# Kernel optimization log

Measured on AMD Instinct MI355X. Metric: run time of the kernel, lower is better.

## Reference

```python
import jax, jax.numpy as jnp
import numpy as np

N_NODES = 50000
SEQ_LEN = 32
N_TOKENS = 100000
EMB_DIM = 128          # in_feats / 2
IN_FEATS = 256
N_HIDDEN = 256
N_CLASSES = 40
N_EDGES = 800000
PAD_IX = 0


def setup_inputs() -> dict:
    key = jax.random.key(0)
    k1, k2, k3, k4, k5, k6 = jax.random.split(key, 6)
    features = jax.random.randint(k1, (N_NODES, SEQ_LEN), 0, N_TOKENS, dtype=jnp.int32)
    src = jax.random.randint(k2, (N_EDGES,), 0, N_NODES, dtype=jnp.int32)
    dst = jax.random.randint(k3, (N_EDGES,), 0, N_NODES, dtype=jnp.int32)
    emb_table = jax.random.normal(k4, (N_TOKENS, EMB_DIM), dtype=jnp.float32) * 0.02
    W1 = jax.random.normal(k5, (IN_FEATS, N_HIDDEN), dtype=jnp.float32) * 0.02
    b1 = jnp.zeros((N_HIDDEN,), dtype=jnp.float32)
    W2 = jax.random.normal(k6, (N_HIDDEN, N_CLASSES), dtype=jnp.float32) * 0.02
    b2 = jnp.zeros((N_CLASSES,), dtype=jnp.float32)
    return {"features": features, "src": src, "dst": dst,
            "emb_table": emb_table, "W1": W1, "b1": b1, "W2": W2, "b2": b2}


def _apply_embs(features, emb_table):
    # padding_idx row contributes zeros (nn.Embedding padding_idx semantics)
    emb = emb_table.at[PAD_IX].set(0.0)
    h = emb[features]                                    # [N, L, D]
    seq_len = jnp.sum(features != PAD_IX, axis=1)        # [N]
    seq_len = jnp.maximum(seq_len, 1)[:, None].astype(h.dtype)
    h1 = h.sum(axis=1) / seq_len                         # masked mean
    h2 = h.max(axis=1)                                   # max pool (pads are 0)
    return jnp.concatenate((h1, h2), axis=1)             # [N, 2D]


def _graph_conv(h, src, dst, norm_s, norm_d, W, b):
    # DGL GraphConv, norm='both': out = D_in^{-1/2} A D_out^{-1/2} h W + b
    hw = h @ W                                           # transform first (smaller msgs)
    m = (hw * norm_s[:, None])[src]                      # gather messages [E, F]
    agg = jax.ops.segment_sum(m, dst, num_segments=N_NODES)
    return agg * norm_d[:, None] + b


def reference(features, src, dst, emb_table, W1, b1, W2, b2):
    ones_e = jnp.ones((src.shape[0],), dtype=jnp.float32)
    deg_out = jnp.maximum(jax.ops.segment_sum(ones_e, src, num_segments=N_NODES), 1.0)
    deg_in = jnp.maximum(jax.ops.segment_sum(ones_e, dst, num_segments=N_NODES), 1.0)
    norm_s = deg_out ** -0.5
    norm_d = deg_in ** -0.5

    h = _apply_embs(features, emb_table)                 # [N, in_feats]
    h = jax.nn.relu(_graph_conv(h, src, dst, norm_s, norm_d, W1, b1))
    # dropout is identity in eval mode
    h = _graph_conv(h, src, dst, norm_s, norm_d, W2, b2)
    return h                                             # [N, n_classes]
```

## Files before the change

kernel.cpp:

```cpp
#include <hip/hip_runtime.h>
#include <math.h>

#define N_NODES 50000
#define SEQ_LEN 32
#define EMB_DIM 128
#define IN_FEATS 256
#define N_HIDDEN 256
#define N_CLASSES 40
#define N_EDGES 800000
#define N_TOKENS 100000

#define SLOT 64
#define NBIN 196
#define BINCAP 4608
#define EPB 4000

typedef short short8 __attribute__((ext_vector_type(8)));
typedef float f32x4 __attribute__((ext_vector_type(4)));
typedef float f32x8 __attribute__((ext_vector_type(8)));

__device__ __forceinline__ unsigned short f2bf(float x) {
  unsigned int u = __float_as_uint(x);
  unsigned int r = (u + 0x7FFFu + ((u >> 16) & 1u)) >> 16;
  return (unsigned short)r;
}
__device__ __forceinline__ float bf2f(unsigned short s) {
  return __uint_as_float((unsigned int)s << 16);
}
__device__ __forceinline__ unsigned int pack2bf(float a, float b) {
  return (unsigned int)f2bf(a) | ((unsigned int)f2bf(b) << 16);
}
__device__ __forceinline__ f32x8 up8(uint4 v) {
  f32x8 f;
  f[0] = __uint_as_float(v.x << 16);
  f[1] = __uint_as_float(v.x & 0xFFFF0000u);
  f[2] = __uint_as_float(v.y << 16);
  f[3] = __uint_as_float(v.y & 0xFFFF0000u);
  f[4] = __uint_as_float(v.z << 16);
  f[5] = __uint_as_float(v.z & 0xFFFF0000u);
  f[6] = __uint_as_float(v.w << 16);
  f[7] = __uint_as_float(v.w & 0xFFFF0000u);
  return f;
}

__global__ __launch_bounds__(256) void k_pre(const int* __restrict__ src,
                                             const int* __restrict__ dst,
                                             int* __restrict__ gcntD,
                                             int* __restrict__ gcntS,
                                             unsigned int* __restrict__ dbin,
                                             unsigned char* __restrict__ sbin,
                                             const float* __restrict__ emb,
                                             unsigned short* __restrict__ emb_b,
                                             const float* __restrict__ W1,
                                             unsigned short* __restrict__ Wp1,
                                             const float* __restrict__ W2,
                                             unsigned short* __restrict__ Wp2) {
  __shared__ int cntD[NBIN], cntS[NBIN], baseD[NBIN], baseS[NBIN];
  int b = blockIdx.x, tid = threadIdx.x;
  if (b < 200) {
    if (tid < NBIN) { cntD[tid] = 0; cntS[tid] = 0; }
    __syncthreads();
    int e0 = b * EPB;
    for (int j = tid; j < EPB; j += 256) {
      int d = dst[e0 + j], s = src[e0 + j];
      atomicAdd(&cntD[d >> 8], 1);
      atomicAdd(&cntS[s >> 8], 1);
    }
    __syncthreads();
    if (tid < NBIN) {
      baseD[tid] = atomicAdd(&gcntD[tid], cntD[tid]);
      baseS[tid] = atomicAdd(&gcntS[tid], cntS[tid]);
      cntD[tid] = 0;
      cntS[tid] = 0;
    }
    __syncthreads();
    for (int j = tid; j < EPB; j += 256) {
      int d = dst[e0 + j], s = src[e0 + j];
      int bd = d >> 8, bs = s >> 8;
      int od = atomicAdd(&cntD[bd], 1);
      int pd = baseD[bd] + od;
      if (pd < BINCAP) dbin[(size_t)bd * BINCAP + pd] = ((unsigned int)s << 8) | (unsigned int)(d & 255);
      int os = atomicAdd(&cntS[bs], 1);
      int ps = baseS[bs] + os;
      if (ps < BINCAP) sbin[(size_t)bs * BINCAP + ps] = (unsigned char)(s & 255);
    }
  } else if (b < 200 + 2048) {
    const int total = N_TOKENS * EMB_DIM / 4;
    for (int i = (b - 200) * 256 + tid; i < total; i += 2048 * 256) {
      float4 v = ((const float4*)emb)[i];
      ushort4 o;
      o.x = f2bf(v.x); o.y = f2bf(v.y); o.z = f2bf(v.z); o.w = f2bf(v.w);
      ((ushort4*)emb_b)[i] = o;
    }
  } else if (b < 200 + 2048 + 32) {
    int g = (b - 2248) * 256 + tid;
    int lane = g & 63, jb = (g >> 6) & 15, kt = g >> 10;
    int col = jb * 16 + (lane & 15);
    int kbase = kt * 32 + (lane >> 4) * 8;
    unsigned short* o = Wp1 + (size_t)g * 8;
    #pragma unroll
    for (int e = 0; e < 8; ++e) o[e] = f2bf(W1[(size_t)(kbase + e) * N_HIDDEN + col]);
  } else {
    int g = (b - 2280) * 256 + tid;
    if (g < 8 * 3 * 64) {
      int lane = g & 63, jb = (g >> 6) % 3, kt = g / (3 * 64);
      int col = jb * 16 + (lane & 15);
      int kbase = kt * 32 + (lane >> 4) * 8;
      unsigned short* o = Wp2 + (size_t)g * 8;
      #pragma unroll
      for (int e = 0; e < 8; ++e)
        o[e] = (col < N_CLASSES) ? f2bf(W2[(size_t)(kbase + e) * N_CLASSES + col]) : (unsigned short)0;
    }
  }
}

__global__ __launch_bounds__(256) void k_phase2(const unsigned int* __restrict__ dbin,
                                                const int* __restrict__ gcntD,
                                                const unsigned char* __restrict__ sbin,
                                                const int* __restrict__ gcntS,
                                                int* __restrict__ cursor,
                                                int* __restrict__ csr_pad,
                                                float* __restrict__ norm_s,
                                                float* __restrict__ norm_d,
                                                const int* __restrict__ feats,
                                                const uint4* __restrict__ rows4,
                                                uint4* __restrict__ h4) {
  __shared__ int cntD[256], cntS[256];
  int tid = threadIdx.x;
  if (blockIdx.x < NBIN) {
    int b = blockIdx.x;
    cntD[tid] = 0; cntS[tid] = 0;
    __syncthreads();
    int n = min(gcntD[b], BINCAP);
    const unsigned int* bb = dbin + (size_t)b * BINCAP;
    for (int j = tid; j < n; j += 256) {
      unsigned int e = bb[j];
      int lo = e & 255;
      int slot = atomicAdd(&cntD[lo], 1);
      if (slot < SLOT) csr_pad[(size_t)(b * 256 + lo) * SLOT + slot] = (int)(e >> 8);
    }
    int ns = min(gcntS[b], BINCAP);
    const unsigned char* sb = sbin + (size_t)b * BINCAP;
    for (int j = tid; j < ns; j += 256) atomicAdd(&cntS[sb[j]], 1);
    __syncthreads();
    int node = b * 256 + tid;
    if (node < N_NODES) {
      cursor[node] = min(cntD[tid], SLOT);
      norm_d[node] = 1.0f / sqrtf((float)max(cntD[tid], 1));
      norm_s[node] = 1.0f / sqrtf((float)max(cntS[tid], 1));
    }
    return;
  }

  int w = tid >> 6, lane = tid & 63;
  int node = (blockIdx.x - NBIN) * 4 + w;
  int lq = lane & 15, qg = lane >> 4;
  int laneL = lane & 31;

  int tok0 = feats[(size_t)node * SEQ_LEN + laneL];
  unsigned long long bm = __ballot(tok0 != 0);
  int cnt = (int)__popcll(bm & 0xFFFFFFFFull);
  float inv = 1.0f / (float)max(cnt, 1);

  f32x8 s = (f32x8)(0.f);
  f32x8 mx = (f32x8)(-INFINITY);
  #pragma unroll
  for (int t = 0; t < 8; ++t) {
    int tok = __shfl(tok0, t * 4 + qg);
    uint4 v = make_uint4(0u, 0u, 0u, 0u);
    if (tok) v = rows4[(size_t)tok * 16 + lq];
    f32x8 f = up8(v);
    s += f;
    mx = __builtin_elementwise_max(mx, f);
  }
  #pragma unroll
  for (int mask = 16; mask <= 32; mask <<= 1) {
    #pragma unroll
    for (int j = 0; j < 8; ++j) {
      s[j] += __shfl_xor(s[j], mask);
      mx[j] = fmaxf(mx[j], __shfl_xor(mx[j], mask));
    }
  }
  if (qg == 0) {
    s *= inv;
    uint4* hv = h4 + (size_t)node * 32;
    hv[lq] = make_uint4(pack2bf(s[0], s[1]), pack2bf(s[2], s[3]),
                        pack2bf(s[4], s[5]), pack2bf(s[6], s[7]));
    hv[16 + lq] = make_uint4(pack2bf(mx[0], mx[1]), pack2bf(mx[2], mx[3]),
                             pack2bf(mx[4], mx[5]), pack2bf(mx[6], mx[7]));
  }
}

__global__ __launch_bounds__(256) void k_mm1(const unsigned short* __restrict__ hb,
                                             const unsigned short* __restrict__ Wp,
                                             const float* __restrict__ norm_s,
                                             unsigned short* __restrict__ out) {
  __shared__ unsigned short sA[64 * 256];
  int tid = threadIdx.x;
  int r0 = blockIdx.x * 64;
  #pragma unroll
  for (int it = 0; it < 8; ++it) {
    int idx = it * 256 + tid;
    int r = idx >> 5, kb = idx & 31;
    uint4 v = make_uint4(0, 0, 0, 0);
    int row = r0 + r;
    if (row < N_NODES) v = *(const uint4*)(hb + (size_t)row * 256 + kb * 8);
    *(uint4*)&sA[r * 256 + ((kb ^ (r & 7)) << 3)] = v;
  }
  __syncthreads();

  int w = tid >> 6, lane = tid & 63;
  const short8* W8 = (const short8*)Wp;
  f32x4 acc[4][4];
  #pragma unroll
  for (int i = 0; i < 4; ++i)
    #pragma unroll
    for (int j = 0; j < 4; ++j) acc[i][j] = (f32x4){0.f, 0.f, 0.f, 0.f};

  #pragma unroll
  for (int kt = 0; kt < 8; ++kt) {
    short8 a[4], b[4];
    int kb = kt * 4 + (lane >> 4);
    #pragma unroll
    for (int ri = 0; ri < 4; ++ri) {
      int r = ri * 16 + (lane & 15);
      a[ri] = *(const short8*)&sA[r * 256 + ((kb ^ (r & 7)) << 3)];
    }
    #pragma unroll
    for (int jb = 0; jb < 4; ++jb) b[jb] = W8[(kt * 16 + w * 4 + jb) * 64 + lane];
    #pragma unroll
    for (int ri = 0; ri < 4; ++ri)
      #pragma unroll
      for (int jb = 0; jb < 4; ++jb)
        acc[ri][jb] = __builtin_amdgcn_mfma_f32_16x16x32_bf16(a[ri], b[jb], acc[ri][jb], 0, 0, 0);
  }

  #pragma unroll
  for (int ri = 0; ri < 4; ++ri) {
    #pragma unroll
    for (int rr = 0; rr < 4; ++rr) {
      int row = r0 + ri * 16 + (lane >> 4) * 4 + rr;
      if (row < N_NODES) {
        float ns = norm_s[row];
        #pragma unroll
        for (int jb = 0; jb < 4; ++jb) {
          int col = w * 64 + jb * 16 + (lane & 15);
          out[(size_t)row * 256 + col] = f2bf(acc[ri][jb][rr] * ns);
        }
      }
    }
  }
}

__global__ __launch_bounds__(256) void k_agg1(const uint4* __restrict__ rows4,
                                              const int* __restrict__ cursor,
                                              const int* __restrict__ csr_pad,
                                              const float* __restrict__ norm_d,
                                              const float* __restrict__ b1,
                                              uint4* __restrict__ out4) {
  int tid = threadIdx.x;
  int w = tid >> 6, lane = tid & 63;
  int node = blockIdx.x * 4 + w;
  int cnt = __builtin_amdgcn_readfirstlane(cursor[node]);
  const int* csr = csr_pad + (size_t)node * SLOT;
  int half = lane >> 5, lq = lane & 31;

  f32x8 a = (f32x8)(0.f);
  int e = 0;
  for (; e + 8 <= cnt; e += 8) {
    int s0 = csr[e + 0 + half], s1 = csr[e + 2 + half];
    int s2 = csr[e + 4 + half], s3 = csr[e + 6 + half];
    uint4 v0 = rows4[(size_t)s0 * 32 + lq];
    uint4 v1 = rows4[(size_t)s1 * 32 + lq];
    uint4 v2 = rows4[(size_t)s2 * 32 + lq];
    uint4 v3 = rows4[(size_t)s3 * 32 + lq];
    a += up8(v0);
    a += up8(v1);
    a += up8(v2);
    a += up8(v3);
  }
  for (; e + 2 <= cnt; e += 2) {
    uint4 v = rows4[(size_t)csr[e + half] * 32 + lq];
    a += up8(v);
  }
  if (e < cnt) {
    uint4 v = make_uint4(0u, 0u, 0u, 0u);
    if (half == 0) v = rows4[(size_t)csr[e] * 32 + lq];
    a += up8(v);
  }
  #pragma unroll
  for (int j = 0; j < 8; ++j) a[j] += __shfl_xor(a[j], 32);

  if (half == 0) {
    float nd = norm_d[node];
    float4 bb0 = *(const float4*)&b1[8 * lq];
    float4 bb1 = *(const float4*)&b1[8 * lq + 4];
    float o0 = fmaxf(a[0] * nd + bb0.x, 0.f), o1 = fmaxf(a[1] * nd + bb0.y, 0.f);
    float o2 = fmaxf(a[2] * nd + bb0.z, 0.f), o3 = fmaxf(a[3] * nd + bb0.w, 0.f);
    float o4 = fmaxf(a[4] * nd + bb1.x, 0.f), o5 = fmaxf(a[5] * nd + bb1.y, 0.f);
    float o6 = fmaxf(a[6] * nd + bb1.z, 0.f), o7 = fmaxf(a[7] * nd + bb1.w, 0.f);
    out4[(size_t)node * 32 + lq] = make_uint4(pack2bf(o0, o1), pack2bf(o2, o3),
                                              pack2bf(o4, o5), pack2bf(o6, o7));
  }
}

__global__ __launch_bounds__(256) void k_mm2(const unsigned short* __restrict__ h2b,
                                             const unsigned short* __restrict__ Wp,
                                             const float* __restrict__ norm_s,
                                             unsigned short* __restrict__ out) {
  __shared__ unsigned short sA[64 * 256];
  int tid = threadIdx.x;
  int r0 = blockIdx.x * 64;
  #pragma unroll
  for (int it = 0; it < 8; ++it) {
    int idx = it * 256 + tid;
    int r = idx >> 5, kb = idx & 31;
    uint4 v = make_uint4(0, 0, 0, 0);
    int row = r0 + r;
    if (row < N_NODES) v = *(const uint4*)(h2b + (size_t)row * 256 + kb * 8);
    *(uint4*)&sA[r * 256 + ((kb ^ (r & 7)) << 3)] = v;
  }
  __syncthreads();

  int w = tid >> 6, lane = tid & 63;
  const short8* W8 = (const short8*)Wp;
  f32x4 acc[3];
  #pragma unroll
  for (int j = 0; j < 3; ++j) acc[j] = (f32x4){0.f, 0.f, 0.f, 0.f};

  #pragma unroll
  for (int kt = 0; kt < 8; ++kt) {
    int r = w * 16 + (lane & 15);
    int kb = kt * 4 + (lane >> 4);
    short8 a = *(const short8*)&sA[r * 256 + ((kb ^ (r & 7)) << 3)];
    #pragma unroll
    for (int jb = 0; jb < 3; ++jb) {
      short8 b = W8[(kt * 3 + jb) * 64 + lane];
      acc[jb] = __builtin_amdgcn_mfma_f32_16x16x32_bf16(a, b, acc[jb], 0, 0, 0);
    }
  }

  #pragma unroll
  for (int rr = 0; rr < 4; ++rr) {
    int row = r0 + w * 16 + (lane >> 4) * 4 + rr;
    if (row < N_NODES) {
      float ns = norm_s[row];
      #pragma unroll
      for (int jb = 0; jb < 3; ++jb) {
        int col = jb * 16 + (lane & 15);
        if (col < N_CLASSES) out[(size_t)row * N_CLASSES + col] = f2bf(acc[jb][rr] * ns);
      }
    }
  }
}

__global__ __launch_bounds__(256) void k_agg2(const uint2* __restrict__ rows2,
                                              const int* __restrict__ cursor,
                                              const int* __restrict__ csr_pad,
                                              const float* __restrict__ norm_d,
                                              const float* __restrict__ b2,
                                              float* __restrict__ out) {
  int tid = threadIdx.x;
  int w = tid >> 6, lane = tid & 63;
  int node = blockIdx.x * 4 + w;
  int slot = lane / 10, fl = lane % 10;
  int cnt = __builtin_amdgcn_readfirstlane(cursor[node]);
  const int* csr = csr_pad + (size_t)node * SLOT;

  float a0 = 0.f, a1 = 0.f, a2 = 0.f, a3 = 0.f;
  if (slot < 6) {
    for (int e = slot; e < cnt; e += 6) {
      int s = csr[e];
      uint2 v = rows2[(size_t)s * 10 + fl];
      a0 += bf2f((unsigned short)(v.x & 0xFFFF));
      a1 += bf2f((unsigned short)(v.x >> 16));
      a2 += bf2f((unsigned short)(v.y & 0xFFFF));
      a3 += bf2f((unsigned short)(v.y >> 16));
    }
  }
  float r10_0 = __shfl(a0, lane + 10), r10_1 = __shfl(a1, lane + 10), r10_2 = __shfl(a2, lane + 10), r10_3 = __shfl(a3, lane + 10);
  float r20_0 = __shfl(a0, lane + 20), r20_1 = __shfl(a1, lane + 20), r20_2 = __shfl(a2, lane + 20), r20_3 = __shfl(a3, lane + 20);
  float r30_0 = __shfl(a0, lane + 30), r30_1 = __shfl(a1, lane + 30), r30_2 = __shfl(a2, lane + 30), r30_3 = __shfl(a3, lane + 30);
  float r40_0 = __shfl(a0, lane + 40), r40_1 = __shfl(a1, lane + 40), r40_2 = __shfl(a2, lane + 40), r40_3 = __shfl(a3, lane + 40);
  float r50_0 = __shfl(a0, lane + 50), r50_1 = __shfl(a1, lane + 50), r50_2 = __shfl(a2, lane + 50), r50_3 = __shfl(a3, lane + 50);
  if (slot == 0) {
    a0 += r10_0 + r20_0 + r30_0 + r40_0 + r50_0;
    a1 += r10_1 + r20_1 + r30_1 + r40_1 + r50_1;
    a2 += r10_2 + r20_2 + r30_2 + r40_2 + r50_2;
    a3 += r10_3 + r20_3 + r30_3 + r40_3 + r50_3;
    float nd = norm_d[node];
    float4 bb = *(const float4*)&b2[4 * fl];
    float4 o = make_float4(a0 * nd + bb.x, a1 * nd + bb.y, a2 * nd + bb.z, a3 * nd + bb.w);
    *(float4*)&out[(size_t)node * N_CLASSES + 4 * fl] = o;
  }
}

extern "C" void kernel_launch(void* const* d_in, const int* in_sizes, int n_in,
                              void* d_out, int out_size, void* d_ws, size_t ws_size,
                              hipStream_t stream) {
  const int*   feats = (const int*)d_in[0];
  const int*   src   = (const int*)d_in[1];
  const int*   dst   = (const int*)d_in[2];
  const float* emb   = (const float*)d_in[3];
  const float* W1    = (const float*)d_in[4];
  const float* b1    = (const float*)d_in[5];
  const float* W2    = (const float*)d_in[6];
  const float* b2    = (const float*)d_in[7];
  float* out = (float*)d_out;

  char* base = (char*)d_ws;
  size_t off = 0;
  auto alloc = [&](size_t bytes) -> char* {
    char* p = base + off;
    off += (bytes + 255) & ~(size_t)255;
    return p;
  };
  unsigned short* hb      = (unsigned short*)alloc((size_t)N_NODES * IN_FEATS * 2);
  unsigned short* msgb    = (unsigned short*)alloc((size_t)N_NODES * N_HIDDEN * 2);
  unsigned short* hw2b    = (unsigned short*)alloc((size_t)N_NODES * N_CLASSES * 2);
  unsigned short* emb_b   = (unsigned short*)alloc((size_t)N_TOKENS * EMB_DIM * 2);
  unsigned short* Wp1     = (unsigned short*)alloc((size_t)8 * 16 * 64 * 8 * 2);
  unsigned short* Wp2     = (unsigned short*)alloc((size_t)8 * 3 * 64 * 8 * 2);
  int*   gcnt    = (int*)alloc((size_t)512 * 4);
  int*   gcntD   = gcnt;
  int*   gcntS   = gcnt + 256;
  int*   cursor  = (int*)alloc((size_t)N_NODES * 4);
  float* norm_s  = (float*)alloc((size_t)N_NODES * 4);
  float* norm_d  = (float*)alloc((size_t)N_NODES * 4);
  unsigned int*  dbin = (unsigned int*)alloc((size_t)NBIN * BINCAP * 4);
  unsigned char* sbin = (unsigned char*)alloc((size_t)NBIN * BINCAP);
  int*   csr_pad = (int*)alloc((size_t)N_NODES * SLOT * 4);

  hipMemsetAsync(gcnt, 0, 512 * 4, stream);

  k_pre<<<200 + 2048 + 32 + 6, 256, 0, stream>>>(src, dst, gcntD, gcntS, dbin, sbin,
                                                 emb, emb_b, W1, Wp1, W2, Wp2);
  k_phase2<<<NBIN + N_NODES / 4, 256, 0, stream>>>(dbin, gcntD, sbin, gcntS, cursor, csr_pad,
                                                   norm_s, norm_d,
                                                   feats, (const uint4*)emb_b, (uint4*)hb);

  int gemm_blocks = (N_NODES + 63) / 64;
  k_mm1<<<gemm_blocks, 256, 0, stream>>>(hb, Wp1, norm_s, msgb);
  k_agg1<<<N_NODES / 4, 256, 0, stream>>>((const uint4*)msgb, cursor, csr_pad, norm_d, b1, (uint4*)hb);
  k_mm2<<<gemm_blocks, 256, 0, stream>>>(hb, Wp2, norm_s, hw2b);
  k_agg2<<<N_NODES / 4, 256, 0, stream>>>((const uint2*)hw2b, cursor, csr_pad, norm_d, b2, out);
}
```

Baseline: 203.1 us.

## Aggregate before first transform and fuse both GEMMs into one kernel

Reorders layer 1 so neighbour aggregation runs on the input features first, with norm_s applied per gathered source inside the aggregation loop. The W1 GEMM, bias and ReLU are then fused with the W2 GEMM in one kernel, which keeps the hidden tile in shared memory. This removes one kernel launch and the global write and reread of the hidden activations. The cost is an extra norm_s gather per edge, a doubled shared-memory footprint per block that may lower occupancy, and one added bf16 rounding of the aggregated input.

```diff
diff --git a/kernel.cpp b/kernel.cpp
--- a/kernel.cpp
+++ b/kernel.cpp
@@ -191,72 +191,11 @@
   }
 }
 
-__global__ __launch_bounds__(256) void k_mm1(const unsigned short* __restrict__ hb,
-                                             const unsigned short* __restrict__ Wp,
-                                             const float* __restrict__ norm_s,
-                                             unsigned short* __restrict__ out) {
-  __shared__ unsigned short sA[64 * 256];
-  int tid = threadIdx.x;
-  int r0 = blockIdx.x * 64;
-  #pragma unroll
-  for (int it = 0; it < 8; ++it) {
-    int idx = it * 256 + tid;
-    int r = idx >> 5, kb = idx & 31;
-    uint4 v = make_uint4(0, 0, 0, 0);
-    int row = r0 + r;
-    if (row < N_NODES) v = *(const uint4*)(hb + (size_t)row * 256 + kb * 8);
-    *(uint4*)&sA[r * 256 + ((kb ^ (r & 7)) << 3)] = v;
-  }
-  __syncthreads();
-
-  int w = tid >> 6, lane = tid & 63;
-  const short8* W8 = (const short8*)Wp;
-  f32x4 acc[4][4];
-  #pragma unroll
-  for (int i = 0; i < 4; ++i)
-    #pragma unroll
-    for (int j = 0; j < 4; ++j) acc[i][j] = (f32x4){0.f, 0.f, 0.f, 0.f};
-
-  #pragma unroll
-  for (int kt = 0; kt < 8; ++kt) {
-    short8 a[4], b[4];
-    int kb = kt * 4 + (lane >> 4);
-    #pragma unroll
-    for (int ri = 0; ri < 4; ++ri) {
-      int r = ri * 16 + (lane & 15);
-      a[ri] = *(const short8*)&sA[r * 256 + ((kb ^ (r & 7)) << 3)];
-    }
-    #pragma unroll
-    for (int jb = 0; jb < 4; ++jb) b[jb] = W8[(kt * 16 + w * 4 + jb) * 64 + lane];
-    #pragma unroll
-    for (int ri = 0; ri < 4; ++ri)
-      #pragma unroll
-      for (int jb = 0; jb < 4; ++jb)
-        acc[ri][jb] = __builtin_amdgcn_mfma_f32_16x16x32_bf16(a[ri], b[jb], acc[ri][jb], 0, 0, 0);
-  }
-
-  #pragma unroll
-  for (int ri = 0; ri < 4; ++ri) {
-    #pragma unroll
-    for (int rr = 0; rr < 4; ++rr) {
-      int row = r0 + ri * 16 + (lane >> 4) * 4 + rr;
-      if (row < N_NODES) {
-        float ns = norm_s[row];
-        #pragma unroll
-        for (int jb = 0; jb < 4; ++jb) {
-          int col = w * 64 + jb * 16 + (lane & 15);
-          out[(size_t)row * 256 + col] = f2bf(acc[ri][jb][rr] * ns);
-        }
-      }
-    }
-  }
-}
-
-__global__ __launch_bounds__(256) void k_agg1(const uint4* __restrict__ rows4,
+__global__ __launch_bounds__(256) void k_aggh(const uint4* __restrict__ rows4,
                                               const int* __restrict__ cursor,
                                               const int* __restrict__ csr_pad,
+                                              const float* __restrict__ norm_s,
                                               const float* __restrict__ norm_d,
-                                              const float* __restrict__ b1,
                                               uint4* __restrict__ out4) {
   int tid = threadIdx.x;
   int w = tid >> 6, lane = tid & 63;
@@ -270,73 +209,116 @@
   for (; e + 8 <= cnt; e += 8) {
     int s0 = csr[e + 0 + half], s1 = csr[e + 2 + half];
     int s2 = csr[e + 4 + half], s3 = csr[e + 6 + half];
+    float n0 = norm_s[s0], n1 = norm_s[s1], n2 = norm_s[s2], n3 = norm_s[s3];
     uint4 v0 = rows4[(size_t)s0 * 32 + lq];
     uint4 v1 = rows4[(size_t)s1 * 32 + lq];
     uint4 v2 = rows4[(size_t)s2 * 32 + lq];
     uint4 v3 = rows4[(size_t)s3 * 32 + lq];
-    a += up8(v0);
-    a += up8(v1);
-    a += up8(v2);
-    a += up8(v3);
+    a += up8(v0) * n0;
+    a += up8(v1) * n1;
+    a += up8(v2) * n2;
+    a += up8(v3) * n3;
   }
   for (; e + 2 <= cnt; e += 2) {
-    uint4 v = rows4[(size_t)csr[e + half] * 32 + lq];
-    a += up8(v);
+    int s = csr[e + half];
+    a += up8(rows4[(size_t)s * 32 + lq]) * norm_s[s];
   }
   if (e < cnt) {
-    uint4 v = make_uint4(0u, 0u, 0u, 0u);
-    if (half == 0) v = rows4[(size_t)csr[e] * 32 + lq];
-    a += up8(v);
+    if (half == 0) {
+      int s = csr[e];
+      a += up8(rows4[(size_t)s * 32 + lq]) * norm_s[s];
+    }
   }
   #pragma unroll
   for (int j = 0; j < 8; ++j) a[j] += __shfl_xor(a[j], 32);
 
   if (half == 0) {
-    float nd = norm_d[node];
-    float4 bb0 = *(const float4*)&b1[8 * lq];
-    float4 bb1 = *(const float4*)&b1[8 * lq + 4];
-    float o0 = fmaxf(a[0] * nd + bb0.x, 0.f), o1 = fmaxf(a[1] * nd + bb0.y, 0.f);
-    float o2 = fmaxf(a[2] * nd + bb0.z, 0.f), o3 = fmaxf(a[3] * nd + bb0.w, 0.f);
-    float o4 = fmaxf(a[4] * nd + bb1.x, 0.f), o5 = fmaxf(a[5] * nd + bb1.y, 0.f);
-    float o6 = fmaxf(a[6] * nd + bb1.z, 0.f), o7 = fmaxf(a[7] * nd + bb1.w, 0.f);
-    out4[(size_t)node * 32 + lq] = make_uint4(pack2bf(o0, o1), pack2bf(o2, o3),
-                                              pack2bf(o4, o5), pack2bf(o6, o7));
-  }
-}
-
-__global__ __launch_bounds__(256) void k_mm2(const unsigned short* __restrict__ h2b,
-                                             const unsigned short* __restrict__ Wp,
-                                             const float* __restrict__ norm_s,
-                                             unsigned short* __restrict__ out) {
+    a *= norm_d[node];
+    out4[(size_t)node * 32 + lq] = make_uint4(pack2bf(a[0], a[1]), pack2bf(a[2], a[3]),
+                                              pack2bf(a[4], a[5]), pack2bf(a[6], a[7]));
+  }
+}
+
+__global__ __launch_bounds__(256) void k_mm12(const unsigned short* __restrict__ ah,
+                                              const unsigned short* __restrict__ Wp1,
+                                              const unsigned short* __restrict__ Wp2,
+                                              const float* __restrict__ b1,
+                                              const float* __restrict__ norm_s,
+                                              unsigned short* __restrict__ out) {
   __shared__ unsigned short sA[64 * 256];
+  __shared__ unsigned short sB[64 * 256];
   int tid = threadIdx.x;
   int r0 = blockIdx.x * 64;
+  int w = tid >> 6, lane = tid & 63;
+
   #pragma unroll
   for (int it = 0; it < 8; ++it) {
     int idx = it * 256 + tid;
     int r = idx >> 5, kb = idx & 31;
     uint4 v = make_uint4(0, 0, 0, 0);
     int row = r0 + r;
-    if (row < N_NODES) v = *(const uint4*)(h2b + (size_t)row * 256 + kb * 8);
+    if (row < N_NODES) v = *(const uint4*)(ah + (size_t)row * 256 + kb * 8);
     *(uint4*)&sA[r * 256 + ((kb ^ (r & 7)) << 3)] = v;
   }
   __syncthreads();
 
-  int w = tid >> 6, lane = tid & 63;
-  const short8* W8 = (const short8*)Wp;
-  f32x4 acc[3];
-  #pragma unroll
-  for (int j = 0; j < 3; ++j) acc[j] = (f32x4){0.f, 0.f, 0.f, 0.f};
+  const short8* W8 = (const short8*)Wp1;
+  f32x4 acc[4][4];
+  #pragma unroll
+  for (int i = 0; i < 4; ++i)
+    #pragma unroll
+    for (int j = 0; j < 4; ++j) acc[i][j] = (f32x4){0.f, 0.f, 0.f, 0.f};
+
+  #pragma unroll
+  for (int kt = 0; kt < 8; ++kt) {
+    short8 a[4], bv[4];
+    int kb = kt * 4 + (lane >> 4);
+    #pragma unroll
+    for (int ri = 0; ri < 4; ++ri) {
+      int r = ri * 16 + (lane & 15);
+      a[ri] = *(const short8*)&sA[r * 256 + ((kb ^ (r & 7)) << 3)];
+    }
+    #pragma unroll
+    for (int jb = 0; jb < 4; ++jb) bv[jb] = W8[(kt * 16 + w * 4 + jb) * 64 + lane];
+    #pragma unroll
+    for (int ri = 0; ri < 4; ++ri)
+      #pragma unroll
+      for (int jb = 0; jb < 4; ++jb)
+        acc[ri][jb] = __builtin_amdgcn_mfma_f32_16x16x32_bf16(a[ri], bv[jb], acc[ri][jb], 0, 0, 0);
+  }
+
+  float bb[4];
+  #pragma unroll
+  for (int jb = 0; jb < 4; ++jb) bb[jb] = b1[w * 64 + jb * 16 + (lane & 15)];
+  #pragma unroll
+  for (int ri = 0; ri < 4; ++ri) {
+    #pragma unroll
+    for (int rr = 0; rr < 4; ++rr) {
+      int r = ri * 16 + (lane >> 4) * 4 + rr;
+      #pragma unroll
+      for (int jb = 0; jb < 4; ++jb) {
+        int col = w * 64 + jb * 16 + (lane & 15);
+        float v = fmaxf(acc[ri][jb][rr] + bb[jb], 0.f);
+        sB[r * 256 + (((col >> 3) ^ (r & 7)) << 3) + (col & 7)] = f2bf(v);
+      }
+    }
+  }
+  __syncthreads();
+
+  const short8* V8 = (const short8*)Wp2;
+  f32x4 acc2[3];
+  #pragma unroll
+  for (int j = 0; j < 3; ++j) acc2[j] = (f32x4){0.f, 0.f, 0.f, 0.f};
 
   #pragma unroll
   for (int kt = 0; kt < 8; ++kt) {
     int r = w * 16 + (lane & 15);
     int kb = kt * 4 + (lane >> 4);
-    short8 a = *(const short8*)&sA[r * 256 + ((kb ^ (r & 7)) << 3)];
+    short8 a = *(const short8*)&sB[r * 256 + ((kb ^ (r & 7)) << 3)];
     #pragma unroll
     for (int jb = 0; jb < 3; ++jb) {
-      short8 b = W8[(kt * 3 + jb) * 64 + lane];
-      acc[jb] = __builtin_amdgcn_mfma_f32_16x16x32_bf16(a, b, acc[jb], 0, 0, 0);
+      short8 bv = V8[(kt * 3 + jb) * 64 + lane];
+      acc2[jb] = __builtin_amdgcn_mfma_f32_16x16x32_bf16(a, bv, acc2[jb], 0, 0, 0);
     }
   }
 
@@ -348,7 +330,7 @@
       #pragma unroll
       for (int jb = 0; jb < 3; ++jb) {
         int col = jb * 16 + (lane & 15);
-        if (col < N_CLASSES) out[(size_t)row * N_CLASSES + col] = f2bf(acc[jb][rr] * ns);
+        if (col < N_CLASSES) out[(size_t)row * N_CLASSES + col] = f2bf(acc2[jb][rr] * ns);
       }
     }
   }
@@ -416,7 +398,7 @@
     return p;
   };
   unsigned short* hb      = (unsigned short*)alloc((size_t)N_NODES * IN_FEATS * 2);
-  unsigned short* msgb    = (unsigned short*)alloc((size_t)N_NODES * N_HIDDEN * 2);
+  unsigned short* ah      = (unsigned short*)alloc((size_t)N_NODES * IN_FEATS * 2);
   unsigned short* hw2b    = (unsigned short*)alloc((size_t)N_NODES * N_CLASSES * 2);
   unsigned short* emb_b   = (unsigned short*)alloc((size_t)N_TOKENS * EMB_DIM * 2);
   unsigned short* Wp1     = (unsigned short*)alloc((size_t)8 * 16 * 64 * 8 * 2);
@@ -440,8 +422,7 @@
                                                    feats, (const uint4*)emb_b, (uint4*)hb);
 
   int gemm_blocks = (N_NODES + 63) / 64;
-  k_mm1<<<gemm_blocks, 256, 0, stream>>>(hb, Wp1, norm_s, msgb);
-  k_agg1<<<N_NODES / 4, 256, 0, stream>>>((const uint4*)msgb, cursor, csr_pad, norm_d, b1, (uint4*)hb);
-  k_mm2<<<gemm_blocks, 256, 0, stream>>>(hb, Wp2, norm_s, hw2b);
+  k_aggh<<<N_NODES / 4, 256, 0, stream>>>((const uint4*)hb, cursor, csr_pad, norm_s, norm_d, (uint4*)ah);
+  k_mm12<<<gemm_blocks, 256, 0, stream>>>(ah, Wp1, Wp2, b1, norm_s, hw2b);
   k_agg2<<<N_NODES / 4, 256, 0, stream>>>((const uint2*)hw2b, cursor, csr_pad, norm_d, b2, out);
 }
```

Measured after the change: 202.1 us. No clear change (-0.5%).
